# Kernel optimization log

Hardware: AMD Instinct MI355X
Metric: run time of the kernel (lower is better)

## Reference

```python
import jax, jax.numpy as jnp
import numpy as np

OBS = 64      # observation_dim = numel of one frame (1*8*8)
EXTRA = 20    # extra_hidden_dim
HID = OBS + EXTRA  # 84
T = 64        # sequence length
B = 16        # batch
L2 = 1e-3     # l2_regularization


def setup_inputs() -> dict:
    key = jax.random.key(0)
    k1, k2, k3 = jax.random.split(key, 3)
    # xavier_uniform-style init for A and C
    A = jax.random.uniform(k1, (HID, HID), minval=-1.0, maxval=1.0) * np.sqrt(6.0 / (HID + HID))
    C = jax.random.uniform(k2, (OBS, HID), minval=-1.0, maxval=1.0) * np.sqrt(6.0 / (OBS + HID))
    x = jax.random.normal(k3, (B, T, 1, 8, 8), dtype=jnp.float32)
    return {"x": x, "A": A.astype(jnp.float32), "C": C.astype(jnp.float32), "step": 0}


def build_M(A, C, seq_len):
    # T_reg = C with l2 added on its leading 'diagonal' entries C[k,k]
    d = jnp.arange(OBS)
    Treg = C.at[d, d].add(L2)
    # blocks[k] = Treg @ A^k, computed by a single scan (no Python loop over T^2)
    def step(carry, _):
        return carry @ A, carry
    _, blocks = jax.lax.scan(step, Treg, None, length=seq_len)  # [T, OBS, HID]
    i = jnp.arange(seq_len)
    diff = i[:, None] - i[None, :]                               # block (i,j) -> A-power i-j
    Mb = jnp.where((diff >= 0)[:, :, None, None],
                   blocks[jnp.clip(diff, 0, seq_len - 1)], 0.0)  # [T, T, OBS, HID]
    # block layout -> dense [T*OBS, T*HID]
    return Mb.transpose(0, 2, 1, 3).reshape(seq_len * OBS, seq_len * HID)


def reference(x, A, C, step):
    Bsz, seq_len = x.shape[0], x.shape[1]
    M = build_M(A, C, seq_len)                   # [T*OBS, T*HID]
    MMT = M @ M.T                                # [T*OBS, T*OBS]
    U = jnp.linalg.cholesky(MMT)                 # lower, as torch.potrf(upper=False)
    # The flow is an external invertible network; surrogate: identity flow, loss = 0
    zcat = x.reshape(Bsz, -1)                    # [B, T*OBS]
    Y = zcat
    z = jax.scipy.linalg.solve_triangular(U, Y.T, lower=True)          # U z = Y^T
    z = jax.scipy.linalg.solve_triangular(U, z, lower=True, trans='T')  # U^T z = z
    xe = (M.T @ z).T                             # [B, T*HID]
    eps = xe[:, HID:]                            # drop first hidden block
    prediction_loss = jnp.mean(eps * eps)        # + flow loss (0 for identity surrogate)
    return prediction_loss
```

## Files before the change

kernel.cpp:

```cpp
#include <hip/hip_runtime.h>

#define OBS 64
#define EXT 20
#define HID 84
#define TT  64
#define BB  16

#define OFF_T1INV 0
#define OFF_XT    4096
#define OFF_NA1   5376
#define OFF_ANT1  6656
#define OFF_ANA1  7936
#define OFF_N     9216
#define OFF_AN    10896
#define OFF_D     12576
#define OFF_DLAST 12976
#define OFF_F     13376
#define OFF_Q     13776
#define OFF_G     79312
#define OFF_JG    99792
#define OFF_ZG    125392
#define OFF_TS    150992
#define OFF_PART  171472
#define OFF_ICONV OFF_D

#define RDLANE(v, l) __uint_as_float(__builtin_amdgcn_readlane((int)__float_as_uint(v), (l)))

__device__ __forceinline__ void ld20(const float* p, float a[20]) {
    const float4* q = (const float4*)p;
    float4 v0 = q[0], v1 = q[1], v2 = q[2], v3 = q[3], v4 = q[4];
    a[0]=v0.x; a[1]=v0.y; a[2]=v0.z; a[3]=v0.w;
    a[4]=v1.x; a[5]=v1.y; a[6]=v1.z; a[7]=v1.w;
    a[8]=v2.x; a[9]=v2.y; a[10]=v2.z; a[11]=v2.w;
    a[12]=v3.x; a[13]=v3.y; a[14]=v3.z; a[15]=v3.w;
    a[16]=v4.x; a[17]=v4.y; a[18]=v4.z; a[19]=v4.w;
}

__device__ __forceinline__ float dot20(const float a[20], const float v[20]) {
    float s0 = 0.f, s1 = 0.f, s2 = 0.f, s3 = 0.f;
    #pragma unroll
    for (int m = 0; m < 20; m += 4) {
        s0 += a[m]     * v[m];
        s1 += a[m + 1] * v[m + 1];
        s2 += a[m + 2] * v[m + 2];
        s3 += a[m + 3] * v[m + 3];
    }
    return (s0 + s1) + (s2 + s3);
}

__global__ __launch_bounds__(64, 1) void k_prepgj(const float* __restrict__ C,
                                                  float* __restrict__ ws) {
    int lane = threadIdx.x;
    float w[64], wi[64];
    #pragma unroll
    for (int c = 0; c < 64; ++c) {
        w[c]  = C[lane * HID + c] + (c == lane ? 1e-3f : 0.0f);
        wi[c] = (c == lane) ? 1.0f : 0.0f;
    }

    bool used = false;
    int myk = 0;
    #pragma unroll 64
    for (int k = 0; k < 64; ++k) {
        float a_rk = w[k];
        float v = used ? -1.0f : fabsf(a_rk);
        int idx = lane;
        #pragma unroll
        for (int off = 32; off; off >>= 1) {
            float v2 = __shfl_down(v, off);
            int   i2 = __shfl_down(idx, off);
            if (v2 > v) { v = v2; idx = i2; }
        }
        int p = __shfl(idx, 0);
        float piv = RDLANE(a_rk, p);
        float rp  = 1.0f / piv;
        bool isp  = (lane == p);
        float fc    = isp ? 0.0f : a_rk * rp;
        float coeff = isp ? rp : -fc;
        if (isp) { used = true; myk = k; }
        #pragma unroll
        for (int c = k + 1; c < 64; ++c) {
            float tmp  = RDLANE(w[c], p);
            float base = isp ? 0.0f : w[c];
            w[c] = fmaf(tmp, coeff, base);
        }
        #pragma unroll
        for (int c = 0; c < 64; ++c) {
            float tmp  = RDLANE(wi[c], p);
            float base = isp ? 0.0f : wi[c];
            wi[c] = fmaf(tmp, coeff, base);
        }
    }

    float* dst = ws + OFF_T1INV + myk * 64;
    #pragma unroll
    for (int c = 0; c < 64; c += 4) {
        float4 v4 = make_float4(wi[c], wi[c + 1], wi[c + 2], wi[c + 3]);
        *reinterpret_cast<float4*>(dst + c) = v4;
    }
}

__global__ __launch_bounds__(512) void k_small(const float* __restrict__ A,
                                               const float* __restrict__ C,
                                               float* __restrict__ ws) {
    __shared__ float Xs[64][20];
    __shared__ float Ns[84][20];
    __shared__ float ANs[84][20];
    int tid = threadIdx.x;

    for (int id = tid; id < 64 * 20; id += 512) {
        int r = id / 20, j = id % 20;
        float s = 0.f;
        const float* tr = ws + OFF_T1INV + r * 64;
        for (int c = 0; c < 64; ++c) s += tr[c] * C[c * HID + 64 + j];
        Xs[r][j] = s;
        ws[OFF_XT + j * 64 + r] = s;
    }
    __syncthreads();
    for (int id = tid; id < HID * 20; id += 512) {
        int p = id / 20, j = id % 20;
        float v = (p < 64) ? -Xs[p][j] : ((p - 64) == j ? 1.f : 0.f);
        Ns[p][j] = v;
        ws[OFF_N + id] = v;
    }
    __syncthreads();
    for (int id = tid; id < HID * 20; id += 512) {
        int p = id / 20, j = id % 20;
        float s = 0.f;
        for (int m = 0; m < HID; ++m) s += A[p * HID + m] * Ns[m][j];
        ANs[p][j] = s;
        ws[OFF_AN + id] = s;
    }
    __syncthreads();
    for (int id = tid; id < 400; id += 512) {
        int a = id / 20, b = id % 20;
        float sn = 0.f, sf = 0.f, sg = 0.f;
        for (int p = 0; p < HID; ++p) {
            sn += Ns[p][a] * Ns[p][b];
            sf += Ns[p][a] * ANs[p][b];
            sg += ANs[p][a] * ANs[p][b];
        }
        ws[OFF_F + id]     = sf;
        ws[OFF_D + id]     = sn + sg;
        ws[OFF_DLAST + id] = sn;
    }
    for (int id = tid; id < 20 * 64; id += 512) {
        int j = id / 64, c = id % 64;
        float s1 = 0.f, s2 = 0.f;
        for (int p = 0; p < HID; ++p) {
            float av = A[p * HID + c];
            s1 += Ns[p][j] * av;
            s2 += ANs[p][j] * av;
        }
        ws[OFF_NA1 + id]  = s1;
        ws[OFF_ANA1 + id] = s2;
        ws[OFF_ANT1 + id] = ANs[c][j];
    }
}

__global__ __launch_bounds__(64, 1) void k_factor(float* __restrict__ ws) {
    __shared__ float sD[400], sDl[400], sF[400];
    int lane = threadIdx.x;
    for (int id = lane; id < 400; id += 64) {
        sD[id]  = ws[OFF_D + id];
        sDl[id] = ws[OFF_DLAST + id];
        sF[id]  = ws[OFF_F + id];
    }
    __syncthreads();

    float* Jg = ws + OFF_JG;
    float* Zg = ws + OFF_ZG;

    float Kprev[20];
    #pragma unroll
    for (int r = 0; r < 20; ++r) Kprev[r] = 0.f;
    int iconv = 62;
    for (int i = 0; i < 64; ++i) {
        bool last = (i == 63);
        float w[40];
        #pragma unroll
        for (int r = 0; r < 20; ++r) {
            float v, v2 = 0.f;
            if (lane < 20) {
                float dv = last ? sDl[r * 20 + lane] : sD[r * 20 + lane];
                v  = dv - Kprev[r];
                v2 = sF[r * 20 + lane];
            } else if (lane < 40) {
                v = sF[(lane - 20) * 20 + r];
            } else if (lane < 60) {
                v = (r == lane - 40) ? 1.f : 0.f;
            } else {
                v = 0.f;
            }
            w[r]      = v;
            w[20 + r] = v2;
        }
        #pragma unroll
        for (int k = 0; k < 20; ++k) {
            float rp = __builtin_amdgcn_rcpf(RDLANE(w[k], k));
            w[k] *= rp;
            #pragma unroll
            for (int r = 0; r < 40; ++r) {
                if (r == k) continue;
                float ck = RDLANE(w[r], k);
                w[r] -= ck * w[k];
            }
        }
        if (lane >= 40 && lane < 60) {
            int c = lane - 40;
            #pragma unroll
            for (int r = 0; r < 20; ++r) {
                Jg[i * 400 + r * 20 + c] = w[r];
                if (!last) Zg[i * 400 + c * 20 + r] = -w[20 + r];
            }
        }
        if (last) break;
        float dmax = 0.f, kmax = 0.f;
        int gsel = (20 + lane) << 2;
        #pragma unroll
        for (int r = 0; r < 20; ++r) {
            float kn = -__uint_as_float(__builtin_amdgcn_ds_bpermute(
                gsel, (int)__float_as_uint(w[20 + r])));
            dmax = fmaxf(dmax, fabsf(kn - Kprev[r]));
            kmax = fmaxf(kmax, fabsf(kn));
            Kprev[r] = kn;
        }
        if (i < 62 && __all((lane >= 20) || (dmax <= 1e-7f + 1e-4f * kmax))) {
            iconv = i;
            i = 62;
        }
    }
    if (lane == 0) ws[OFF_ICONV] = __int_as_float(iconv);
}

__global__ __launch_bounds__(64) void k_qg(const float* __restrict__ x,
                                           float* __restrict__ ws) {
    int i = blockIdx.x, b = blockIdx.y, r = threadIdx.x;
    __shared__ float yv[3][64];
    __shared__ float qs[3][64];
    yv[1][r] = x[(b * TT + i) * 64 + r];
    yv[0][r] = (i > 0)  ? x[(b * TT + i - 1) * 64 + r] : 0.f;
    yv[2][r] = (i < 63) ? x[(b * TT + i + 1) * 64 + r] : 0.f;
    __syncthreads();
    const float* Ti = ws + OFF_T1INV + r * 64;
    float q0 = 0.f, q1 = 0.f, q2 = 0.f;
    for (int c = 0; c < 64; ++c) {
        float t = Ti[c];
        q0 += t * yv[0][c];
        q1 += t * yv[1][c];
        q2 += t * yv[2][c];
    }
    qs[0][r] = q0; qs[1][r] = q1; qs[2][r] = q2;
    ws[OFF_Q + (b * TT + i) * 64 + r] = q1;
    __syncthreads();
    if (r < 20) {
        const float* xt = ws + OFF_XT   + r * 64;
        const float* na = ws + OFF_NA1  + r * 64;
        const float* at = ws + OFF_ANT1 + r * 64;
        const float* aa = ws + OFF_ANA1 + r * 64;
        float s = 0.f;
        if (i < 63) {
            for (int c = 0; c < 64; ++c)
                s += xt[c] * qs[1][c] + na[c] * qs[0][c] + at[c] * qs[2][c] - aa[c] * qs[1][c];
        } else {
            for (int c = 0; c < 64; ++c)
                s += xt[c] * qs[1][c] + na[c] * qs[0][c];
        }
        ws[OFF_G + (i * 16 + b) * 20 + r] = s;
    }
}

__global__ __launch_bounds__(64, 1) void k_sweeps(float* __restrict__ ws) {
    __shared__ float rh[TT][2][20];
    __shared__ float th[2][20];
    int lane = threadIdx.x;
    int bh   = lane >> 5;
    int b    = (blockIdx.x << 1) + bh;
    int j    = lane & 31;
    int jj   = (j < 20) ? j : 0;
    bool actj = (j < 20);

    int icv = __float_as_int(ws[OFF_ICONV]);
    const float* G  = ws + OFF_G;
    const float* Jg = ws + OFF_JG;
    const float* Zg = ws + OFF_ZG;
    float* TS = ws + OFF_TS;

    float Mrow[20];
    #pragma unroll
    for (int m = 0; m < 20; ++m) Mrow[m] = Zg[icv * 400 + m * 20 + jj];
    float Jr[20], Zr[20], J63r[20];
    ld20(Jg + icv * 400 + jj * 20, Jr);
    ld20(Zg + icv * 400 + jj * 20, Zr);
    ld20(Jg + 63 * 400 + jj * 20, J63r);

    float rt = 0.f, gnext = 0.f;
    if (actj) {
        rt    = G[(0 * 16 + b) * 20 + j];
        rh[0][bh][j] = rt;
        gnext = G[(1 * 16 + b) * 20 + j];
    }
    for (int i = 1; i < TT; ++i) {
        float rv[20];
        ld20(&rh[i - 1][bh][0], rv);
        float s;
        if (i - 1 < icv) {
            float fr[20];
            #pragma unroll
            for (int m = 0; m < 20; ++m) fr[m] = Zg[(i - 1) * 400 + m * 20 + jj];
            s = gnext + dot20(fr, rv);
        } else {
            s = gnext + dot20(Mrow, rv);
        }
        rt = s;
        if (actj) {
            rh[i][bh][j] = rt;
            gnext = (i + 1 < TT) ? G[((i + 1) * 16 + b) * 20 + j] : 0.f;
        }
    }

    {
        float rv[20];
        ld20(&rh[63][bh][0], rv);
        float tn = dot20(J63r, rv);
        if (actj) {
            TS[(63 * 16 + b) * 20 + j] = tn;
            th[bh][j] = tn;
        }
        for (int i = 62; i >= 0; --i) {
            float rvi[20], tv[20];
            ld20(&rh[i][bh][0], rvi);
            ld20(&th[bh][0], tv);
            float t;
            if (i < icv) {
                float jr[20], zr[20];
                ld20(Jg + i * 400 + jj * 20, jr);
                ld20(Zg + i * 400 + jj * 20, zr);
                t = dot20(jr, rvi) + dot20(zr, tv);
            } else {
                t = dot20(Jr, rvi) + dot20(Zr, tv);
            }
            if (actj) {
                TS[(i * 16 + b) * 20 + j] = t;
                th[bh][j] = t;
            }
        }
    }
}

__global__ __launch_bounds__(128) void k_loss(const float* __restrict__ A,
                                              float* __restrict__ ws) {
    int i = blockIdx.x + 1, b = blockIdx.y, tid = threadIdx.x;
    __shared__ float ti[20], tm[20], qi[64], qm[64];
    __shared__ float red[128];
    if (tid < 20) {
        ti[tid] = ws[OFF_TS + (i * 16 + b) * 20 + tid];
        tm[tid] = ws[OFF_TS + ((i - 1) * 16 + b) * 20 + tid];
    }
    if (tid < 64) {
        qi[tid] = ws[OFF_Q + (b * TT + i) * 64 + tid];
        qm[tid] = ws[OFF_Q + (b * TT + i - 1) * 64 + tid];
    }
    __syncthreads();
    float e = 0.f;
    if (tid < HID) {
        int p = tid;
        float s = (p < 64) ? qi[p] : 0.f;
        const float* Np  = ws + OFF_N  + p * 20;
        const float* ANp = ws + OFF_AN + p * 20;
        for (int j = 0; j < 20; ++j) s += Np[j] * ti[j] - ANp[j] * tm[j];
        const float* Ar = A + p * HID;
        for (int c = 0; c < 64; ++c) s -= Ar[c] * qm[c];
        e = s * s;
    }
    red[tid] = e;
    __syncthreads();
    for (int off = 64; off; off >>= 1) {
        if (tid < off) red[tid] += red[tid + off];
        __syncthreads();
    }
    if (tid == 0) ws[OFF_PART + b * 63 + (i - 1)] = red[0];
}

__global__ __launch_bounds__(256) void k_reduce(const float* __restrict__ ws,
                                                float* __restrict__ out) {
    __shared__ float red[256];
    int tid = threadIdx.x;
    float s = 0.f;
    for (int id = tid; id < BB * 63; id += 256) s += ws[OFF_PART + id];
    red[tid] = s;
    __syncthreads();
    for (int off = 128; off; off >>= 1) {
        if (tid < off) red[tid] += red[tid + off];
        __syncthreads();
    }
    if (tid == 0) out[0] = red[0] / (float)(BB * (TT - 1) * HID);
}

extern "C" void kernel_launch(void* const* d_in, const int* in_sizes, int n_in,
                              void* d_out, int out_size, void* d_ws, size_t ws_size,
                              hipStream_t stream) {
    (void)in_sizes; (void)n_in; (void)out_size; (void)ws_size;
    const float* x = (const float*)d_in[0];
    const float* A = (const float*)d_in[1];
    const float* C = (const float*)d_in[2];
    float* ws  = (float*)d_ws;
    float* out = (float*)d_out;

    k_prepgj<<<dim3(1),          dim3(64),  0, stream>>>(C, ws);
    k_small <<<dim3(1),          dim3(512), 0, stream>>>(A, C, ws);
    k_factor<<<dim3(1),          dim3(64),  0, stream>>>(ws);
    k_qg    <<<dim3(TT, BB),     dim3(64),  0, stream>>>(x, ws);
    k_sweeps<<<dim3(8),          dim3(64),  0, stream>>>(ws);
    k_loss  <<<dim3(TT - 1, BB), dim3(128), 0, stream>>>(A, ws);
    k_reduce<<<dim3(1),          dim3(256), 0, stream>>>(ws, out);
}
```

Before: 231.7 us.

## Invert 64x64 block via 2x2 Schur complement and fuse into prep kernel

Result: faster. 185.9 us (-19.8%).

```diff
diff --git a/kernel.cpp b/kernel.cpp
--- a/kernel.cpp
+++ b/kernel.cpp
@@ -48,65 +48,142 @@
     return (s0 + s1) + (s2 + s3);
 }
 
-__global__ __launch_bounds__(64, 1) void k_prepgj(const float* __restrict__ C,
-                                                  float* __restrict__ ws) {
-    int lane = threadIdx.x;
-    float w[64], wi[64];
-    #pragma unroll
-    for (int c = 0; c < 64; ++c) {
-        w[c]  = C[lane * HID + c] + (c == lane ? 1e-3f : 0.0f);
-        wi[c] = (c == lane) ? 1.0f : 0.0f;
-    }
-
-    bool used = false;
-    int myk = 0;
-    #pragma unroll 64
-    for (int k = 0; k < 64; ++k) {
-        float a_rk = w[k];
-        float v = used ? -1.0f : fabsf(a_rk);
-        int idx = lane;
-        #pragma unroll
-        for (int off = 32; off; off >>= 1) {
-            float v2 = __shfl_down(v, off);
-            int   i2 = __shfl_down(idx, off);
-            if (v2 > v) { v = v2; idx = i2; }
-        }
-        int p = __shfl(idx, 0);
-        float piv = RDLANE(a_rk, p);
-        float rp  = 1.0f / piv;
-        bool isp  = (lane == p);
-        float fc    = isp ? 0.0f : a_rk * rp;
-        float coeff = isp ? rp : -fc;
-        if (isp) { used = true; myk = k; }
-        #pragma unroll
-        for (int c = k + 1; c < 64; ++c) {
-            float tmp  = RDLANE(w[c], p);
-            float base = isp ? 0.0f : w[c];
-            w[c] = fmaf(tmp, coeff, base);
-        }
-        #pragma unroll
-        for (int c = 0; c < 64; ++c) {
-            float tmp  = RDLANE(wi[c], p);
-            float base = isp ? 0.0f : wi[c];
-            wi[c] = fmaf(tmp, coeff, base);
-        }
-    }
-
-    float* dst = ws + OFF_T1INV + myk * 64;
-    #pragma unroll
-    for (int c = 0; c < 64; c += 4) {
-        float4 v4 = make_float4(wi[c], wi[c + 1], wi[c + 2], wi[c + 3]);
-        *reinterpret_cast<float4*>(dst + c) = v4;
-    }
-}
-
-__global__ __launch_bounds__(512) void k_small(const float* __restrict__ A,
-                                               const float* __restrict__ C,
-                                               float* __restrict__ ws) {
+__global__ __launch_bounds__(512) void k_prep(const float* __restrict__ A,
+                                              const float* __restrict__ C,
+                                              float* __restrict__ ws) {
+    __shared__ float sPinv[1024], sW[1024], sV[1024], sSc[1024];
+    __shared__ float sScinv[1024], sX1[1024], sX2[1024];
     __shared__ float Xs[64][20];
     __shared__ float Ns[84][20];
     __shared__ float ANs[84][20];
-    int tid = threadIdx.x;
+    int tid = threadIdx.x, wave = tid >> 6, lane = tid & 63;
+
+    if (wave == 0 && lane < 32) {
+        float w[32], wi[32];
+        #pragma unroll
+        for (int c = 0; c < 32; ++c) {
+            w[c]  = C[lane * HID + c] + (c == lane ? 1e-3f : 0.0f);
+            wi[c] = (c == lane) ? 1.0f : 0.0f;
+        }
+        bool used = false; int myk = 0;
+        #pragma unroll
+        for (int k = 0; k < 32; ++k) {
+            float a_rk = w[k];
+            float v = used ? -1.0f : fabsf(a_rk);
+            int idx = lane;
+            #pragma unroll
+            for (int off = 16; off; off >>= 1) {
+                float v2 = __shfl_down(v, off, 32);
+                int   i2 = __shfl_down(idx, off, 32);
+                if (v2 > v) { v = v2; idx = i2; }
+            }
+            int p = __shfl(idx, 0, 32);
+            float piv = RDLANE(a_rk, p);
+            float rp  = 1.0f / piv;
+            bool isp  = (lane == p);
+            float coeff = isp ? rp : -(a_rk * rp);
+            if (isp) { used = true; myk = k; }
+            #pragma unroll
+            for (int c = k + 1; c < 32; ++c) {
+                float tmp = RDLANE(w[c], p);
+                w[c] = fmaf(tmp, coeff, isp ? 0.0f : w[c]);
+            }
+            #pragma unroll
+            for (int c = 0; c < 32; ++c) {
+                float tmp = RDLANE(wi[c], p);
+                wi[c] = fmaf(tmp, coeff, isp ? 0.0f : wi[c]);
+            }
+        }
+        #pragma unroll
+        for (int c = 0; c < 32; ++c) sPinv[myk * 32 + c] = wi[c];
+    }
+    __syncthreads();
+
+    for (int id = tid; id < 2048; id += 512) {
+        int sel = id >> 10, rc = id & 1023, r = rc >> 5, c = rc & 31;
+        float s = 0.f;
+        if (sel == 0) {
+            for (int m = 0; m < 32; ++m) s += C[(32 + r) * HID + m] * sPinv[m * 32 + c];
+            sW[rc] = s;
+        } else {
+            for (int m = 0; m < 32; ++m) s += sPinv[r * 32 + m] * C[m * HID + 32 + c];
+            sV[rc] = s;
+        }
+    }
+    __syncthreads();
+
+    for (int id = tid; id < 1024; id += 512) {
+        int r = id >> 5, c = id & 31;
+        float s = C[(32 + r) * HID + 32 + c] + (r == c ? 1e-3f : 0.f);
+        for (int m = 0; m < 32; ++m) s -= sW[r * 32 + m] * C[m * HID + 32 + c];
+        sSc[id] = s;
+    }
+    __syncthreads();
+
+    if (wave == 0 && lane < 32) {
+        float w[32], wi[32];
+        #pragma unroll
+        for (int c = 0; c < 32; ++c) {
+            w[c]  = sSc[lane * 32 + c];
+            wi[c] = (c == lane) ? 1.0f : 0.0f;
+        }
+        bool used = false; int myk = 0;
+        #pragma unroll
+        for (int k = 0; k < 32; ++k) {
+            float a_rk = w[k];
+            float v = used ? -1.0f : fabsf(a_rk);
+            int idx = lane;
+            #pragma unroll
+            for (int off = 16; off; off >>= 1) {
+                float v2 = __shfl_down(v, off, 32);
+                int   i2 = __shfl_down(idx, off, 32);
+                if (v2 > v) { v = v2; idx = i2; }
+            }
+            int p = __shfl(idx, 0, 32);
+            float piv = RDLANE(a_rk, p);
+            float rp  = 1.0f / piv;
+            bool isp  = (lane == p);
+            float coeff = isp ? rp : -(a_rk * rp);
+            if (isp) { used = true; myk = k; }
+            #pragma unroll
+            for (int c = k + 1; c < 32; ++c) {
+                float tmp = RDLANE(w[c], p);
+                w[c] = fmaf(tmp, coeff, isp ? 0.0f : w[c]);
+            }
+            #pragma unroll
+            for (int c = 0; c < 32; ++c) {
+                float tmp = RDLANE(wi[c], p);
+                wi[c] = fmaf(tmp, coeff, isp ? 0.0f : wi[c]);
+            }
+        }
+        #pragma unroll
+        for (int c = 0; c < 32; ++c) sScinv[myk * 32 + c] = wi[c];
+    }
+    __syncthreads();
+
+    for (int id = tid; id < 2048; id += 512) {
+        int sel = id >> 10, rc = id & 1023, r = rc >> 5, c = rc & 31;
+        float s = 0.f;
+        if (sel == 0) {
+            for (int m = 0; m < 32; ++m) s += sScinv[r * 32 + m] * sW[m * 32 + c];
+            sX1[rc] = s;
+        } else {
+            for (int m = 0; m < 32; ++m) s += sV[r * 32 + m] * sScinv[m * 32 + c];
+            sX2[rc] = s;
+        }
+    }
+    __syncthreads();
+
+    for (int id = tid; id < 1024; id += 512) {
+        int r = id >> 5, c = id & 31;
+        float x3 = 0.f;
+        for (int m = 0; m < 32; ++m) x3 += sV[r * 32 + m] * sX1[m * 32 + c];
+        ws[OFF_T1INV + r * 64 + c]              = sPinv[id] + x3;
+        ws[OFF_T1INV + r * 64 + 32 + c]         = -sX2[id];
+        ws[OFF_T1INV + (32 + r) * 64 + c]       = -sX1[id];
+        ws[OFF_T1INV + (32 + r) * 64 + 32 + c]  = sScinv[id];
+    }
+    __syncthreads();
 
     for (int id = tid; id < 64 * 20; id += 512) {
         int r = id / 20, j = id % 20;
@@ -407,8 +484,7 @@
     float* ws  = (float*)d_ws;
     float* out = (float*)d_out;
 
-    k_prepgj<<<dim3(1),          dim3(64),  0, stream>>>(C, ws);
-    k_small <<<dim3(1),          dim3(512), 0, stream>>>(A, C, ws);
+    k_prep  <<<dim3(1),          dim3(512), 0, stream>>>(A, C, ws);
     k_factor<<<dim3(1),          dim3(64),  0, stream>>>(ws);
     k_qg    <<<dim3(TT, BB),     dim3(64),  0, stream>>>(x, ws);
     k_sweeps<<<dim3(8),          dim3(64),  0, stream>>>(ws);
```
